# Kernel optimization log

Hardware: AMD Instinct MI355X
Metric: run time of the kernel (lower is better)

## Reference

```python
import jax, jax.numpy as jnp
import numpy as np

# H2RConfig constants
KERNEL = 3
MAX_ROUTES = 1000
STRIDE = 4.0
MIN_SIZE = 32.0
MAX_SIZE = 512.0
SCORE_POWER = 2.0
UNC_WEIGHT = 0.35


def setup_inputs() -> dict:
    key = jax.random.key(0)
    k1, k2, k3 = jax.random.split(key, 3)
    shape = (32, 1, 512, 512)  # [B, 1, H, W] heatmaps at stride 4
    return {
        "route_logits": jax.random.normal(k1, shape, jnp.float32),
        "scale_logits": jax.random.normal(k2, shape, jnp.float32),
        "uncertainty_logits": jax.random.normal(k3, shape, jnp.float32),
        "image_h": 2048,
        "image_w": 2048,
    }


def reference(route_logits, scale_logits, uncertainty_logits, image_h, image_w):
    # score map: sigmoid^power, modulated by uncertainty (use_route_uncertainty=True)
    score = jnp.power(jax.nn.sigmoid(route_logits), SCORE_POWER)
    score = score * (1.0 - UNC_WEIGHT * jax.nn.sigmoid(uncertainty_logits))

    # local-max NMS: 3x3 max pool, stride 1, SAME padding (torch pads with -inf)
    pooled = jax.lax.reduce_window(
        score, -jnp.inf, jax.lax.max,
        window_dimensions=(1, 1, KERNEL, KERNEL),
        window_strides=(1, 1, 1, 1),
        padding="SAME",
    )
    peak_mask = score == pooled
    filtered = jnp.where(peak_mask, score, -1.0)

    B = score.shape[0]
    Wd = score.shape[3]
    flat = filtered.reshape(B, -1)                 # [B, H*W]
    values, indices = jax.lax.top_k(flat, MAX_ROUTES)  # [B, K]
    valid = values > 0.0                            # torch drops these; we mask/pad

    ys = indices // Wd
    xs = indices % Wd
    cx = (xs.astype(jnp.float32) + 0.5) * STRIDE
    cy = (ys.astype(jnp.float32) + 0.5) * STRIDE

    # gather scale / uncertainty at peak locations
    sc = jnp.take_along_axis(scale_logits.reshape(B, -1), indices, axis=1)
    un = jax.nn.sigmoid(jnp.take_along_axis(uncertainty_logits.reshape(B, -1), indices, axis=1))

    side = MIN_SIZE + jax.nn.sigmoid(sc) * (MAX_SIZE - MIN_SIZE)
    side = side * (1.0 + 0.25 * un)
    half = side * 0.5

    iw = float(image_w)
    ih = float(image_h)
    x1 = jnp.clip(cx - half, 0.0, iw - 1.0)
    y1 = jnp.clip(cy - half, 0.0, ih - 1.0)
    x2 = jnp.clip(cx + half, 1.0, iw)
    y2 = jnp.clip(cy + half, 1.0, ih)

    bcol = jnp.broadcast_to(jnp.arange(B, dtype=jnp.float32)[:, None], values.shape)
    rois = jnp.stack([bcol, x1, y1, x2, y2], axis=-1)  # [B, K, 5]

    # padded (fixed-shape) equivalent of torch's variable-length concat
    rois = jnp.where(valid[..., None], rois, 0.0)
    scores = jnp.where(valid, values, 0.0)
    return rois, scores, valid
```

## Files before the change

### kernel.cpp

```cpp
#include <hip/hip_runtime.h>
#include <hip/hip_bf16.h>
#include <math.h>


#define B_   32
#define H_   512
#define W_   512
#define HW_  (H_ * W_)
#define K_   1000
#define ROWS_ 16
#define THR_  512
#define NSTRIP_ 32
#define WSEGCAP_ 176
#define STRIPCAP_ (8 * WSEGCAP_)
#define NSLOT_ (NSTRIP_ * STRIPCAP_)
#define NPAIR_ (NSLOT_ / 2)
#define NBUK_ 4096
#define NW2_  (NBUK_ / 2)
#define GCAP_ 2048

#define PL_BYTES_  ((size_t)B_ * NSLOT_ * 8)
#define GH2_BYTES_ ((size_t)B_ * NSTRIP_ * NW2_ * 4)

__device__ __forceinline__ float np_expf(float x) {
#pragma clang fp contract(off)
    const float log2e = 1.44269504088896341f;
    float z = x * log2e;
    float m = rintf(z);
    float r = fmaf(m, -0.693359375f, x);
    r = fmaf(m, 2.12194440e-4f, r);
    float r2 = r * r;
    float p = fmaf(1.9875691500e-4f, r, 1.3981999507e-3f);
    p = fmaf(p, r, 8.3334519073e-3f);
    p = fmaf(p, r, 4.1665795894e-2f);
    p = fmaf(p, r, 1.6666665459e-1f);
    p = fmaf(p, r, 5.0000001201e-1f);
    p = fmaf(p, r2, r);
    p = p + 1.0f;
    int mi = (int)m;
    float sc = __int_as_float((127 + mi) << 23);
    return p * sc;
}

__device__ __forceinline__ float sigmoid_np(float x) {
#pragma clang fp contract(off)
    float e = np_expf(-x);
    float d = 1.0f + e;
    return 1.0f / d;
}

__device__ __forceinline__ float score_ref(float r, float u) {
#pragma clang fp contract(off)
    float s  = sigmoid_np(r);
    float s2 = s * s;
    float su = sigmoid_np(u);
    float t  = 0.35f * su;
    float m  = 1.0f - t;
    return s2 * m;
}

__device__ __forceinline__ float sigmoid_fast(float x) {
    return 1.0f / (1.0f + __expf(-x));
}

__global__ __launch_bounds__(THR_, 4) void fused_peak_kernel(
    const float* __restrict__ route, const float* __restrict__ unc,
    unsigned long long* __restrict__ plist,
    unsigned int* __restrict__ ghist2)
{
    __shared__ float sm[ROWS_ + 2][W_];

    const int tid   = threadIdx.x;
    const int lane  = tid & 63;
    const int wid   = tid >> 6;
    const int strip = blockIdx.x;
    const int b     = blockIdx.y;
    const int r0    = strip * ROWS_;

    const float4* rb4 = (const float4*)(route + (size_t)b * HW_);
    const float4* ub4 = (const float4*)(unc   + (size_t)b * HW_);
    unsigned long long* wseg =
        plist + (size_t)(b * NSTRIP_ + strip) * STRIPCAP_ + wid * WSEGCAP_;

    float4 rv[5], uv[5];
    int lrow[5], c4[5]; bool ok[5];
    #pragma unroll
    for (int k = 0; k < 5; ++k) {
        int slot = tid + k * THR_;
        slot = slot < 2303 ? slot : 2303;
        int row = slot >> 7;
        int gy  = r0 - 1 + row;
        lrow[k] = row; c4[k] = slot & 127;
        ok[k]   = (gy >= 0 && gy < H_);
        int cy  = gy < 0 ? 0 : (gy >= H_ ? H_ - 1 : gy);
        rv[k] = rb4[cy * 128 + c4[k]];
        uv[k] = ub4[cy * 128 + c4[k]];
    }
    #pragma unroll
    for (int k = 0; k < 5; ++k) {
        float4 s;
        s.x = score_ref(rv[k].x, uv[k].x);
        s.y = score_ref(rv[k].y, uv[k].y);
        s.z = score_ref(rv[k].z, uv[k].z);
        s.w = score_ref(rv[k].w, uv[k].w);
        if (!ok[k]) { s.x = -INFINITY; s.y = -INFINITY;
                      s.z = -INFINITY; s.w = -INFINITY; }
        *(float4*)&sm[lrow[k]][c4[k] * 4] = s;
    }
    __syncthreads();

    const unsigned long long lt = (1ull << lane) - 1ull;
    int wn = 0;
    unsigned int hreg[8];
    #pragma unroll
    for (int j = 0; j < 4; ++j) {
        int g  = tid + j * THR_;
        int ly = 1 + (g >> 7);
        int x0 = (g & 127) * 4;
        int gy = r0 + (ly - 1);
        float4 q0 = *(const float4*)&sm[ly - 1][x0];
        float4 q1 = *(const float4*)&sm[ly    ][x0];
        float4 q2 = *(const float4*)&sm[ly + 1][x0];
        bool hasL = (x0 > 0), hasR = (x0 + 4 < W_);
        float l0 = hasL ? sm[ly - 1][x0 - 1] : -INFINITY;
        float l1 = hasL ? sm[ly    ][x0 - 1] : -INFINITY;
        float l2 = hasL ? sm[ly + 1][x0 - 1] : -INFINITY;
        float e0 = hasR ? sm[ly - 1][x0 + 4] : -INFINITY;
        float e1 = hasR ? sm[ly    ][x0 + 4] : -INFINITY;
        float e2 = hasR ? sm[ly + 1][x0 + 4] : -INFINITY;
        float f_m1 = fmaxf(l0, fmaxf(l1, l2));
        float f_0  = fmaxf(q0.x, fmaxf(q1.x, q2.x));
        float f_1  = fmaxf(q0.y, fmaxf(q1.y, q2.y));
        float f_2  = fmaxf(q0.z, fmaxf(q1.z, q2.z));
        float f_3  = fmaxf(q0.w, fmaxf(q1.w, q2.w));
        float f_4  = fmaxf(e0, fmaxf(e1, e2));
        float tb0  = fmaxf(q0.x, q2.x);
        float tb1  = fmaxf(q0.y, q2.y);
        float tb2  = fmaxf(q0.z, q2.z);
        float tb3  = fmaxf(q0.w, q2.w);
        float vv[4] = { q1.x, q1.y, q1.z, q1.w };
        float mm[4];
        mm[0] = fmaxf(fmaxf(f_m1, f_1), tb0);
        mm[1] = fmaxf(fmaxf(f_0,  f_2), tb1);
        mm[2] = fmaxf(fmaxf(f_1,  f_3), tb2);
        mm[3] = fmaxf(fmaxf(f_2,  f_4), tb3);
        unsigned int pk01 = 0u, pk23 = 0u;
        #pragma unroll
        for (int i = 0; i < 4; ++i) {
            bool take = (vv[i] >= mm[i]);
            unsigned long long mk = __ballot(take);
            if (take) {
                int p = wn + __popcll(mk & lt);
                if (p < WSEGCAP_) {
                    unsigned int bits = __float_as_uint(vv[i]);
                    unsigned int idx  = (unsigned int)(gy * W_ + x0 + i);
                    wseg[p] = ((unsigned long long)bits << 32)
                              | (0xFFFFFFFFu - idx);
                    unsigned int bkt = bits >> 18;
                    if (i < 2) pk01 |= bkt << (16 * i);
                    else       pk23 |= bkt << (16 * (i - 2));
                }
            }
            wn += __popcll(mk);
        }
        hreg[2 * j]     = pk01;
        hreg[2 * j + 1] = pk23;
    }
    for (int i = (wn < WSEGCAP_ ? wn : WSEGCAP_) + lane; i < WSEGCAP_; i += 64)
        wseg[i] = 0ull;
    __syncthreads();

    unsigned int* hist = (unsigned int*)&sm[0][0];
    for (int i = tid; i < NW2_; i += THR_) hist[i] = 0u;
    __syncthreads();

    #pragma unroll
    for (int j = 0; j < 8; ++j) {
        unsigned int h  = hreg[j];
        unsigned int b0 = h & 0xFFFFu;
        unsigned int b1 = h >> 16;
        if (b0) atomicAdd(&hist[b0 >> 1], 1u << ((b0 & 1) * 16));
        if (b1) atomicAdd(&hist[b1 >> 1], 1u << ((b1 & 1) * 16));
    }
    __syncthreads();

    unsigned int* gh2 = ghist2 + (size_t)(b * NSTRIP_ + strip) * NW2_;
    for (int i = tid; i < NW2_; i += THR_) gh2[i] = hist[i];
}

__global__ __launch_bounds__(1024) void select2_kernel(
    const float* __restrict__ scale, const float* __restrict__ unc,
    const unsigned long long* __restrict__ plist,
    const unsigned int* __restrict__ ghist2,
    const int* __restrict__ ih_p, const int* __restrict__ iw_p,
    float* __restrict__ out)
{
    __shared__ unsigned int hist[NBUK_];
    __shared__ unsigned int cursor[NBUK_];
    __shared__ unsigned long long grp[GCAP_];
    __shared__ int sh_T, sh_nc;

    const int b = blockIdx.x, tid = threadIdx.x;
    const int lane = tid & 63, wid = tid >> 6;

    const unsigned int* gbase = ghist2 + (size_t)b * NSTRIP_ * NW2_;
    for (int w = tid; w < NW2_; w += 1024) {
        unsigned int s0 = 0u, s1 = 0u;
        #pragma unroll
        for (int s = 0; s < NSTRIP_; ++s) {
            unsigned int v = gbase[s * NW2_ + w];
            s0 += v & 0xFFFFu;
            s1 += v >> 16;
        }
        hist[2 * w]     = s0;
        hist[2 * w + 1] = s1;
    }
    __syncthreads();

    if (wid == 0) {
        int Tv = 0;
        int total = 0;
        for (int c = NBUK_ / 64 - 1; c >= 0; --c) {
            int cnt = (int)hist[c * 64 + lane];
            int sum = cnt;
            #pragma unroll
            for (int off = 32; off > 0; off >>= 1)
                sum += __shfl_down(sum, off, 64);
            sum = __shfl(sum, 0, 64);
            if (total + sum < K_) { total += sum; continue; }
            int suf = cnt;
            #pragma unroll
            for (int off = 1; off < 64; off <<= 1) {
                int o = __shfl_down(suf, off, 64);
                suf += (lane + off < 64) ? o : 0;
            }
            bool cond = (total + suf) >= K_;
            unsigned long long mask = __ballot(cond);
            int ls = 63 - __builtin_clzll(mask);
            Tv = c * 64 + ls;
            break;
        }
        if (Tv < 1) Tv = 1;

        int run = 0;
        for (int cb = NBUK_ - 64; cb >= (Tv & ~63); cb -= 64) {
            int beta = cb + lane;
            int cnt = (beta >= Tv) ? (int)hist[beta] : 0;
            int suf = cnt;
            #pragma unroll
            for (int off = 1; off < 64; off <<= 1) {
                int o = __shfl_down(suf, off, 64);
                suf += (lane + off < 64) ? o : 0;
            }
            int chunk_total = __shfl(suf, 0, 64);
            if (beta >= Tv) cursor[beta] = (unsigned int)(run + (suf - cnt));
            run += chunk_total;
        }
        if (lane == 0) { sh_T = Tv; sh_nc = run; }
    }
    __syncthreads();
    const unsigned int T = (unsigned int)sh_T;

    {
        const ulonglong2* p2 = (const ulonglong2*)(plist + (size_t)b * NSLOT_);
        for (int i = tid; i < NPAIR_; i += 1024) {
            ulonglong2 a = p2[i];
            unsigned int b0 = (unsigned int)(a.x >> 50);
            unsigned int b1 = (unsigned int)(a.y >> 50);
            if (b0 >= T) {
                unsigned int pos = atomicAdd(&cursor[b0], 1u);
                if (pos < GCAP_) grp[pos] = a.x;
            }
            if (b1 >= T) {
                unsigned int pos = atomicAdd(&cursor[b1], 1u);
                if (pos < GCAP_) grp[pos] = a.y;
            }
        }
    }
    __syncthreads();

    const float fih = (float)(*ih_p);
    const float fiw = (float)(*iw_p);
    float* rois   = out;
    float* scores = out + (size_t)B_ * K_ * 5;
    float* validf = out + (size_t)B_ * K_ * 6;

    int nc = sh_nc;
    int ncEff = nc < GCAP_ ? nc : GCAP_;
    for (int p = tid; p < ncEff; p += 1024) {
        unsigned long long key = grp[p];
        unsigned int beta = (unsigned int)(key >> 50);
        int segEnd   = (int)cursor[beta];
        int segStart = segEnd - (int)hist[beta];
        int qEnd = segEnd < GCAP_ ? segEnd : GCAP_;
        int r = 0;
        for (int q = segStart; q < qEnd; ++q)
            r += (grp[q] > key) ? 1 : 0;
        int rank = segStart + r;
        if (rank < K_) {
            int o = b * K_ + rank;
            unsigned int bits = (unsigned int)(key >> 32);
            float v = __uint_as_float(bits);
            unsigned int idx = 0xFFFFFFFFu - (unsigned int)(key & 0xFFFFFFFFull);
            int y = (int)(idx >> 9), x = (int)(idx & 511u);
            float cx = ((float)x + 0.5f) * 4.0f;
            float cy = ((float)y + 0.5f) * 4.0f;
            float ss = sigmoid_fast(scale[(size_t)b * HW_ + idx]);
            float su = sigmoid_fast(unc  [(size_t)b * HW_ + idx]);
            float side = (32.0f + ss * 480.0f) * (1.0f + 0.25f * su);
            float half = 0.5f * side;
            float x1 = fminf(fmaxf(cx - half, 0.0f), fiw - 1.0f);
            float y1 = fminf(fmaxf(cy - half, 0.0f), fih - 1.0f);
            float x2 = fminf(fmaxf(cx + half, 1.0f), fiw);
            float y2 = fminf(fmaxf(cy + half, 1.0f), fih);
            rois[o * 5 + 0] = (float)b;
            rois[o * 5 + 1] = x1; rois[o * 5 + 2] = y1;
            rois[o * 5 + 3] = x2; rois[o * 5 + 4] = y2;
            scores[o] = v; validf[o] = 1.0f;
        }
    }
    for (int k = nc + tid; k < K_; k += 1024) {
        int o = b * K_ + k;
        rois[o * 5 + 0] = 0.0f; rois[o * 5 + 1] = 0.0f;
        rois[o * 5 + 2] = 0.0f; rois[o * 5 + 3] = 0.0f;
        rois[o * 5 + 4] = 0.0f;
        scores[o] = 0.0f; validf[o] = 0.0f;
    }
}

extern "C" void kernel_launch(void* const* d_in, const int* in_sizes, int n_in,
                              void* d_out, int out_size, void* d_ws, size_t ws_size,
                              hipStream_t stream) {
    const float* route = (const float*)d_in[0];
    const float* scale = (const float*)d_in[1];
    const float* unc   = (const float*)d_in[2];
    const int*   ih    = (const int*)d_in[3];
    const int*   iw    = (const int*)d_in[4];
    float* out = (float*)d_out;

    unsigned char* base = (unsigned char*)d_ws;
    unsigned long long* plist = (unsigned long long*)base;
    unsigned int* ghist2 = (unsigned int*)(base + PL_BYTES_);

    dim3 g(NSTRIP_, B_);
    fused_peak_kernel<<<g, THR_, 0, stream>>>(route, unc, plist, ghist2);
    select2_kernel<<<B_, 1024, 0, stream>>>(scale, unc, plist, ghist2,
                                            ih, iw, out);
}
```

Measured before the change: 164.5 us.

## Add hot-candidate list and top-bucket fast path to skip full histogram scan

The peak kernel also writes high-score peaks (float bits at or above a fixed threshold) into a compact per-strip hot list, using a wave-aggregated shared atomic counter. The select kernel first builds only the top 64 histogram buckets from the last words of each strip. If those buckets hold at least K candidates, it selects from the small hot list instead of reducing the full 4096-bucket histogram and scanning the whole peak list. Otherwise it falls back to the original path. This costs an extra ballot, atomic and store per candidate in the peak kernel, plus additional workspace.

```diff
diff --git a/kernel.cpp b/kernel.cpp
--- a/kernel.cpp
+++ b/kernel.cpp
@@ -18,9 +18,13 @@
 #define NBUK_ 4096
 #define NW2_  (NBUK_ / 2)
 #define GCAP_ 2048
+#define HOTCAP_ 896
+#define HOTPAIR_ (NSTRIP_ * HOTCAP_ / 2)
+#define HOTBITS_ 0x3F000000u
 
 #define PL_BYTES_  ((size_t)B_ * NSLOT_ * 8)
 #define GH2_BYTES_ ((size_t)B_ * NSTRIP_ * NW2_ * 4)
+#define HL_BYTES_  ((size_t)B_ * NSTRIP_ * HOTCAP_ * 8)
 
 __device__ __forceinline__ float np_expf(float x) {
 #pragma clang fp contract(off)
@@ -66,9 +70,11 @@
 __global__ __launch_bounds__(THR_, 4) void fused_peak_kernel(
     const float* __restrict__ route, const float* __restrict__ unc,
     unsigned long long* __restrict__ plist,
-    unsigned int* __restrict__ ghist2)
+    unsigned int* __restrict__ ghist2,
+    unsigned long long* __restrict__ hotlist)
 {
     __shared__ float sm[ROWS_ + 2][W_];
+    __shared__ int hcnt;
 
     const int tid   = threadIdx.x;
     const int lane  = tid & 63;
@@ -76,11 +82,14 @@
     const int strip = blockIdx.x;
     const int b     = blockIdx.y;
     const int r0    = strip * ROWS_;
+    if (tid == 0) hcnt = 0;
 
     const float4* rb4 = (const float4*)(route + (size_t)b * HW_);
     const float4* ub4 = (const float4*)(unc   + (size_t)b * HW_);
     unsigned long long* wseg =
         plist + (size_t)(b * NSTRIP_ + strip) * STRIPCAP_ + wid * WSEGCAP_;
+    unsigned long long* hseg =
+        hotlist + (size_t)(b * NSTRIP_ + strip) * HOTCAP_;
 
     float4 rv[5], uv[5];
     int lrow[5], c4[5]; bool ok[5];
@@ -149,16 +158,29 @@
         for (int i = 0; i < 4; ++i) {
             bool take = (vv[i] >= mm[i]);
             unsigned long long mk = __ballot(take);
-            if (take) {
-                int p = wn + __popcll(mk & lt);
-                if (p < WSEGCAP_) {
-                    unsigned int bits = __float_as_uint(vv[i]);
-                    unsigned int idx  = (unsigned int)(gy * W_ + x0 + i);
-                    wseg[p] = ((unsigned long long)bits << 32)
-                              | (0xFFFFFFFFu - idx);
-                    unsigned int bkt = bits >> 18;
-                    if (i < 2) pk01 |= bkt << (16 * i);
-                    else       pk23 |= bkt << (16 * (i - 2));
+            int p = wn + __popcll(mk & lt);
+            bool stored = take && (p < WSEGCAP_);
+            unsigned int bits = __float_as_uint(vv[i]);
+            unsigned long long key = 0ull;
+            if (stored) {
+                unsigned int idx = (unsigned int)(gy * W_ + x0 + i);
+                key = ((unsigned long long)bits << 32)
+                      | (0xFFFFFFFFu - idx);
+                wseg[p] = key;
+                unsigned int bkt = bits >> 18;
+                if (i < 2) pk01 |= bkt << (16 * i);
+                else       pk23 |= bkt << (16 * (i - 2));
+            }
+            bool hot = stored && (bits >= HOTBITS_);
+            unsigned long long hmk = __ballot(hot);
+            if (hmk) {
+                int ldr = __ffsll(hmk) - 1;
+                int hb = 0;
+                if (lane == ldr) hb = atomicAdd(&hcnt, __popcll(hmk));
+                hb = __shfl(hb, ldr, 64);
+                if (hot) {
+                    int hp = hb + __popcll(hmk & lt);
+                    if (hp < HOTCAP_) hseg[hp] = key;
                 }
             }
             wn += __popcll(mk);
@@ -169,6 +191,11 @@
     for (int i = (wn < WSEGCAP_ ? wn : WSEGCAP_) + lane; i < WSEGCAP_; i += 64)
         wseg[i] = 0ull;
     __syncthreads();
+
+    {
+        int hn = hcnt < HOTCAP_ ? hcnt : HOTCAP_;
+        for (int i = hn + tid; i < HOTCAP_; i += THR_) hseg[i] = 0ull;
+    }
 
     unsigned int* hist = (unsigned int*)&sm[0][0];
     for (int i = tid; i < NW2_; i += THR_) hist[i] = 0u;
@@ -192,79 +219,124 @@
     const float* __restrict__ scale, const float* __restrict__ unc,
     const unsigned long long* __restrict__ plist,
     const unsigned int* __restrict__ ghist2,
+    const unsigned long long* __restrict__ hotlist,
     const int* __restrict__ ih_p, const int* __restrict__ iw_p,
     float* __restrict__ out)
 {
     __shared__ unsigned int hist[NBUK_];
     __shared__ unsigned int cursor[NBUK_];
     __shared__ unsigned long long grp[GCAP_];
-    __shared__ int sh_T, sh_nc;
+    __shared__ int sh_T, sh_nc, sh_fb;
 
     const int b = blockIdx.x, tid = threadIdx.x;
     const int lane = tid & 63, wid = tid >> 6;
-
     const unsigned int* gbase = ghist2 + (size_t)b * NSTRIP_ * NW2_;
-    for (int w = tid; w < NW2_; w += 1024) {
-        unsigned int s0 = 0u, s1 = 0u;
+
+    if (tid == 0) { sh_fb = 0; sh_T = 1; sh_nc = 0; }
+    if (tid < 64) hist[NBUK_ - 64 + tid] = 0u;
+    __syncthreads();
+    {
+        int s = tid >> 5;
+        int w = (NW2_ - 32) + (tid & 31);
+        unsigned int v = gbase[(size_t)s * NW2_ + w];
+        int bkt = 2 * w;
+        if (v & 0xFFFFu) atomicAdd(&hist[bkt],     v & 0xFFFFu);
+        if (v >> 16)     atomicAdd(&hist[bkt + 1], v >> 16);
+    }
+    __syncthreads();
+
+    if (wid == 0) {
+        int cnt = (int)hist[NBUK_ - 64 + lane];
+        int sum = cnt;
         #pragma unroll
-        for (int s = 0; s < NSTRIP_; ++s) {
-            unsigned int v = gbase[s * NW2_ + w];
-            s0 += v & 0xFFFFu;
-            s1 += v >> 16;
-        }
-        hist[2 * w]     = s0;
-        hist[2 * w + 1] = s1;
-    }
-    __syncthreads();
-
-    if (wid == 0) {
-        int Tv = 0;
-        int total = 0;
-        for (int c = NBUK_ / 64 - 1; c >= 0; --c) {
-            int cnt = (int)hist[c * 64 + lane];
-            int sum = cnt;
-            #pragma unroll
-            for (int off = 32; off > 0; off >>= 1)
-                sum += __shfl_down(sum, off, 64);
-            sum = __shfl(sum, 0, 64);
-            if (total + sum < K_) { total += sum; continue; }
+        for (int off = 32; off > 0; off >>= 1)
+            sum += __shfl_down(sum, off, 64);
+        sum = __shfl(sum, 0, 64);
+        if (sum < K_) {
+            if (lane == 0) sh_fb = 1;
+        } else {
             int suf = cnt;
             #pragma unroll
             for (int off = 1; off < 64; off <<= 1) {
                 int o = __shfl_down(suf, off, 64);
                 suf += (lane + off < 64) ? o : 0;
             }
-            bool cond = (total + suf) >= K_;
+            bool cond = suf >= K_;
             unsigned long long mask = __ballot(cond);
             int ls = 63 - __builtin_clzll(mask);
-            Tv = c * 64 + ls;
-            break;
-        }
-        if (Tv < 1) Tv = 1;
-
-        int run = 0;
-        for (int cb = NBUK_ - 64; cb >= (Tv & ~63); cb -= 64) {
-            int beta = cb + lane;
-            int cnt = (beta >= Tv) ? (int)hist[beta] : 0;
-            int suf = cnt;
+            int beta = NBUK_ - 64 + lane;
+            if (lane >= ls) cursor[beta] = (unsigned int)(suf - cnt);
+            int ncv = __shfl(suf, ls, 64);
+            if (lane == 0) { sh_T = NBUK_ - 64 + ls; sh_nc = ncv; }
+        }
+    }
+    __syncthreads();
+
+    if (sh_fb) {
+        for (int w = tid; w < NW2_; w += 1024) {
+            unsigned int s0 = 0u, s1 = 0u;
             #pragma unroll
-            for (int off = 1; off < 64; off <<= 1) {
-                int o = __shfl_down(suf, off, 64);
-                suf += (lane + off < 64) ? o : 0;
-            }
-            int chunk_total = __shfl(suf, 0, 64);
-            if (beta >= Tv) cursor[beta] = (unsigned int)(run + (suf - cnt));
-            run += chunk_total;
-        }
-        if (lane == 0) { sh_T = Tv; sh_nc = run; }
+            for (int s = 0; s < NSTRIP_; ++s) {
+                unsigned int v = gbase[s * NW2_ + w];
+                s0 += v & 0xFFFFu;
+                s1 += v >> 16;
+            }
+            hist[2 * w]     = s0;
+            hist[2 * w + 1] = s1;
+        }
+        __syncthreads();
+        if (wid == 0) {
+            int Tv = 0;
+            int total = 0;
+            for (int c = NBUK_ / 64 - 1; c >= 0; --c) {
+                int cnt = (int)hist[c * 64 + lane];
+                int sum = cnt;
+                #pragma unroll
+                for (int off = 32; off > 0; off >>= 1)
+                    sum += __shfl_down(sum, off, 64);
+                sum = __shfl(sum, 0, 64);
+                if (total + sum < K_) { total += sum; continue; }
+                int suf = cnt;
+                #pragma unroll
+                for (int off = 1; off < 64; off <<= 1) {
+                    int o = __shfl_down(suf, off, 64);
+                    suf += (lane + off < 64) ? o : 0;
+                }
+                bool cond = (total + suf) >= K_;
+                unsigned long long mask = __ballot(cond);
+                int ls = 63 - __builtin_clzll(mask);
+                Tv = c * 64 + ls;
+                break;
+            }
+            if (Tv < 1) Tv = 1;
+            int run = 0;
+            for (int cb = NBUK_ - 64; cb >= (Tv & ~63); cb -= 64) {
+                int beta = cb + lane;
+                int cnt = (beta >= Tv) ? (int)hist[beta] : 0;
+                int suf = cnt;
+                #pragma unroll
+                for (int off = 1; off < 64; off <<= 1) {
+                    int o = __shfl_down(suf, off, 64);
+                    suf += (lane + off < 64) ? o : 0;
+                }
+                int chunk_total = __shfl(suf, 0, 64);
+                if (beta >= Tv) cursor[beta] = (unsigned int)(run + (suf - cnt));
+                run += chunk_total;
+            }
+            if (lane == 0) { sh_T = Tv; sh_nc = run; }
+        }
     }
     __syncthreads();
     const unsigned int T = (unsigned int)sh_T;
+    const int fb = sh_fb;
 
     {
-        const ulonglong2* p2 = (const ulonglong2*)(plist + (size_t)b * NSLOT_);
-        for (int i = tid; i < NPAIR_; i += 1024) {
-            ulonglong2 a = p2[i];
+        const ulonglong2* src = fb
+            ? (const ulonglong2*)(plist   + (size_t)b * NSLOT_)
+            : (const ulonglong2*)(hotlist + (size_t)b * NSTRIP_ * HOTCAP_);
+        const int npr = fb ? NPAIR_ : HOTPAIR_;
+        for (int i = tid; i < npr; i += 1024) {
+            ulonglong2 a = src[i];
             unsigned int b0 = (unsigned int)(a.x >> 50);
             unsigned int b1 = (unsigned int)(a.y >> 50);
             if (b0 >= T) {
@@ -341,9 +413,12 @@
     unsigned char* base = (unsigned char*)d_ws;
     unsigned long long* plist = (unsigned long long*)base;
     unsigned int* ghist2 = (unsigned int*)(base + PL_BYTES_);
+    unsigned long long* hotlist =
+        (unsigned long long*)(base + PL_BYTES_ + GH2_BYTES_);
 
     dim3 g(NSTRIP_, B_);
-    fused_peak_kernel<<<g, THR_, 0, stream>>>(route, unc, plist, ghist2);
+    fused_peak_kernel<<<g, THR_, 0, stream>>>(route, unc, plist, ghist2,
+                                              hotlist);
     select2_kernel<<<B_, 1024, 0, stream>>>(scale, unc, plist, ghist2,
-                                            ih, iw, out);
-}
+                                            hotlist, ih, iw, out);
+}
```

Result: no change. 164.6 us (+0.1%).
